# Performance work log

Hardware: AMD Instinct MI355X
Metric: run time of the kernel (lower is better)

## Reference

```python
import jax, jax.numpy as jnp
import numpy as np

N = 16384   # total nodes per drug-batch
E = 65536   # directed edges (avg degree 4)
B = 512     # graphs per batch
BN_EPS = 1e-5
SLOPE = 0.01  # LeakyReLU default


def _rn(k, shape, s=0.02):
    return jax.random.normal(k, shape, dtype=jnp.float32) * s


def setup_inputs():
    key = jax.random.key(0)
    ks = jax.random.split(key, 32)
    d = {}
    d['x1'] = jax.random.normal(ks[0], (N, 78), dtype=jnp.float32)
    d['edge_index1'] = jax.random.randint(ks[1], (2, E), 0, N)
    d['batch1'] = jnp.sort(jax.random.randint(ks[2], (N,), 0, B))
    d['x2'] = jax.random.normal(ks[3], (N, 78), dtype=jnp.float32)
    d['edge_index2'] = jax.random.randint(ks[4], (2, E), 0, N)
    d['batch2'] = jnp.sort(jax.random.randint(ks[5], (N,), 0, B))
    d['cell'] = jax.random.normal(ks[6], (B, 954), dtype=jnp.float32)
    # TransformerConv1: 78 -> 2 heads x 128 (concat 256)
    d['wq1'] = _rn(ks[7], (78, 256));  d['bq1'] = jnp.zeros((256,), jnp.float32)
    d['wk1'] = _rn(ks[8], (78, 256));  d['bk1'] = jnp.zeros((256,), jnp.float32)
    d['wv1'] = _rn(ks[9], (78, 256));  d['bv1'] = jnp.zeros((256,), jnp.float32)
    d['ws1'] = _rn(ks[10], (78, 256)); d['bs1'] = jnp.zeros((256,), jnp.float32)
    # TransformerConv2: 256 -> 2 heads x 512 (concat 1024)
    d['wq2'] = _rn(ks[11], (256, 1024)); d['bq2'] = jnp.zeros((1024,), jnp.float32)
    d['wk2'] = _rn(ks[12], (256, 1024)); d['bk2'] = jnp.zeros((1024,), jnp.float32)
    d['wv2'] = _rn(ks[13], (256, 1024)); d['bv2'] = jnp.zeros((1024,), jnp.float32)
    d['ws2'] = _rn(ks[14], (256, 1024)); d['bs2'] = jnp.zeros((1024,), jnp.float32)
    d['wg1'] = _rn(ks[15], (1024, 512)); d['bg1'] = jnp.zeros((512,), jnp.float32)
    d['wg2'] = _rn(ks[16], (512, 128));  d['bg2'] = jnp.zeros((128,), jnp.float32)
    d['wr1'] = _rn(ks[17], (954, 512));  d['br1'] = jnp.zeros((512,), jnp.float32)
    d['wr2'] = _rn(ks[18], (512, 256));  d['br2'] = jnp.zeros((256,), jnp.float32)
    d['wr3'] = _rn(ks[19], (256, 128));  d['br3'] = jnp.zeros((128,), jnp.float32)
    d['wf1'] = _rn(ks[20], (384, 512));  d['bf1'] = jnp.zeros((512,), jnp.float32)
    d['gbn1'] = jnp.ones((512,), jnp.float32); d['bbn1'] = jnp.zeros((512,), jnp.float32)
    d['wf2'] = _rn(ks[21], (512, 256));  d['bf2'] = jnp.zeros((256,), jnp.float32)
    d['gbn2'] = jnp.ones((256,), jnp.float32); d['bbn2'] = jnp.zeros((256,), jnp.float32)
    d['wf3'] = _rn(ks[22], (256, 1));    d['bf3'] = jnp.zeros((1,), jnp.float32)
    return d


def _lrelu(x):
    return jnp.where(x >= 0, x, SLOPE * x)


def _l2n(x):
    return x / jnp.maximum(jnp.linalg.norm(x, axis=1, keepdims=True), 1e-12)


def _tconv(x, ei, wq, bq, wk, bk, wv, bv, ws, bs, H, D):
    # PyG TransformerConv (concat=True, beta=False, root_weight=True)
    src, dst = ei[0], ei[1]
    n = x.shape[0]
    q = (x @ wq + bq).reshape(n, H, D)
    k = (x @ wk + bk).reshape(n, H, D)
    v = (x @ wv + bv).reshape(n, H, D)
    logits = jnp.einsum('ehd,ehd->eh', q[dst], k[src]) / jnp.sqrt(jnp.float32(D))  # [E,H]
    m = jax.ops.segment_max(logits, dst, num_segments=n)
    m = jnp.where(jnp.isfinite(m), m, 0.0)
    e = jnp.exp(logits - m[dst])
    z = jax.ops.segment_sum(e, dst, num_segments=n)
    alpha = e / (z[dst] + 1e-16)
    agg = jax.ops.segment_sum(alpha[:, :, None] * v[src], dst, num_segments=n)  # [N,H,D]
    return agg.reshape(n, H * D) + x @ ws + bs


def reference(x1, edge_index1, batch1, x2, edge_index2, batch2, cell,
              wq1, bq1, wk1, bk1, wv1, bv1, ws1, bs1,
              wq2, bq2, wk2, bk2, wv2, bv2, ws2, bs2,
              wg1, bg1, wg2, bg2, wr1, br1, wr2, br2, wr3, br3,
              wf1, bf1, gbn1, bbn1, wf2, bf2, gbn2, bbn2, wf3, bf3):
    def branch(x, ei, bt):
        h = _lrelu(_tconv(x, ei, wq1, bq1, wk1, bk1, wv1, bv1, ws1, bs1, 2, 128))
        h = _lrelu(_tconv(h, ei, wq2, bq2, wk2, bk2, wv2, bv2, ws2, bs2, 2, 512))
        g = jax.ops.segment_max(h, bt, num_segments=B)  # global max pool per graph
        g = jnp.where(jnp.isfinite(g), g, 0.0)
        g = _lrelu(g @ wg1 + bg1)
        g = g @ wg2 + bg2  # dropout = identity in eval
        return _l2n(g)

    x1g = branch(x1, edge_index1, batch1)
    x2g = branch(x2, edge_index2, batch2)

    c = _l2n(cell)
    c = _lrelu(c @ wr1 + br1)
    c = _lrelu(c @ wr2 + br2)
    c = c @ wr3 + br3

    xc = _l2n(jnp.concatenate([x1g, x2g, c], axis=1))  # [B, 384]
    bn = 1.0 / jnp.sqrt(1.0 + BN_EPS)  # eval BN with running mean 0, var 1
    h = _lrelu((xc @ wf1 + bf1) * bn * gbn1 + bbn1)
    h = _lrelu((h @ wf2 + bf2) * bn * gbn2 + bbn2)
    return jax.nn.sigmoid((h @ wf3 + bf3)[:, 0])
```

## Files before the change

kernel.cpp:

```cpp
#include <hip/hip_runtime.h>
#include <hip/hip_bf16.h>
#include <hip/hip_fp8.h>
#include <math.h>
#include <stdint.h>

typedef __hip_bfloat16 bf16;

#define NN 16384
#define EE 65536
#define BB 512

typedef __attribute__((ext_vector_type(8))) short short8;
typedef __attribute__((ext_vector_type(4))) short short4v;
typedef __attribute__((ext_vector_type(2))) short short2v;
typedef __attribute__((ext_vector_type(4))) float floatx4;
typedef __attribute__((ext_vector_type(8))) unsigned char uchar8;
typedef __attribute__((ext_vector_type(2))) unsigned char uchar2v;

#define GKEY_NEGINF 0x007FFFFFu

__device__ __forceinline__ float lrelu_f(float x){ return x >= 0.f ? x : 0.01f*x; }

__device__ __forceinline__ float b2f(short s){
    unsigned int u = ((unsigned int)(unsigned short)s) << 16;
    float f; __builtin_memcpy(&f, &u, 4); return f;
}
__device__ __forceinline__ short f2b(float f){
    bf16 b = (bf16)f;
    short s; __builtin_memcpy(&s, &b, 2); return s;
}
__device__ __forceinline__ unsigned char f2fp8(float f){
    __hip_fp8_e4m3 t(f);
    return (unsigned char)t.__x;
}
__device__ __forceinline__ float fp82f(unsigned char c){
    __hip_fp8_e4m3 t; t.__x = (__hip_fp8_storage_t)c;
    return (float)t;
}
__device__ __forceinline__ unsigned int fkey(float f){
    unsigned int u; __builtin_memcpy(&u, &f, 4);
    return (u & 0x80000000u) ? ~u : (u | 0x80000000u);
}
__device__ __forceinline__ float fdec(unsigned int k){
    if (k == GKEY_NEGINF) return 0.f;
    unsigned int u = (k & 0x80000000u) ? (k ^ 0x80000000u) : ~k;
    float f; __builtin_memcpy(&f, &u, 4); return f;
}

__device__ __forceinline__ void gl2lds16(const void* g, void* l){
    __builtin_amdgcn_global_load_lds(
        (__attribute__((address_space(1))) unsigned int*)(uintptr_t)g,
        (__attribute__((address_space(3))) unsigned int*)(uintptr_t)l, 16, 0, 0);
}

__global__ __launch_bounds__(256)
void mfma_gemm(const bf16* __restrict__ A, int lda,
               const bf16* __restrict__ Bt, int ldb,
               const float* __restrict__ bias,
               bf16* __restrict__ C, int ldc,
               unsigned char* __restrict__ C2, int ldc2, int nsplit, int K)
{
    __shared__ __align__(16) char smem[20480];
    bf16* As  = (bf16*)smem;
    bf16* Bs  = (bf16*)(smem + 8192);
    bf16* epi = (bf16*)smem;
    const int tid  = threadIdx.x;
    const int wave = tid >> 6;
    const int lane = tid & 63;
    const int wm = (wave & 1) * 64;
    const int wn = (wave >> 1) * 64;
    const int m0 = blockIdx.y * 128;
    const int n0 = blockIdx.x * 128;
    const bool isf8 = (n0 >= nsplit);

    const int srow = lane >> 2;
    const int scol = (lane & 3) * 8;
    const int arow = lane & 15;
    const int aq   = (lane >> 4) * 8;

    floatx4 acc[4][4];
    #pragma unroll
    for (int i=0;i<4;i++)
        #pragma unroll
        for (int j=0;j<4;j++) acc[i][j] = (floatx4){0.f,0.f,0.f,0.f};

    for (int k0 = 0; k0 < K; k0 += 32) {
        #pragma unroll
        for (int i = 0; i < 2; i++) {
            const int chunk = wave*2 + i;
            const int r = chunk*16 + srow;
            gl2lds16(A  + (size_t)(m0 + r)*lda + k0 + scol, As + chunk*512);
            gl2lds16(Bt + (size_t)(n0 + r)*ldb + k0 + scol, Bs + chunk*512);
        }
        __syncthreads();
        short8 af[4], bf_[4];
        #pragma unroll
        for (int i=0;i<4;i++) af[i]  = *(const short8*)(As + (wm + i*16 + arow)*32 + aq);
        #pragma unroll
        for (int j=0;j<4;j++) bf_[j] = *(const short8*)(Bs + (wn + j*16 + arow)*32 + aq);
        #pragma unroll
        for (int i=0;i<4;i++)
            #pragma unroll
            for (int j=0;j<4;j++)
                acc[i][j] = __builtin_amdgcn_mfma_f32_16x16x32_bf16(af[i], bf_[j], acc[i][j], 0,0,0);
        __syncthreads();
    }
    const int crow = (lane >> 4) * 4;
    const int ccol = lane & 15;
    const int erow = lane >> 2;
    const int ecol = (lane & 3) * 8;
    bf16* ep = epi + wave * (64*40);
    #pragma unroll
    for (int j2 = 0; j2 < 2; j2++){
        if (j2) __syncthreads();
        #pragma unroll
        for (int jj = 0; jj < 2; jj++){
            const int j = j2*2 + jj;
            const float bsv = bias[n0 + wn + j*16 + ccol];
            #pragma unroll
            for (int i = 0; i < 4; i++)
                #pragma unroll
                for (int r = 0; r < 4; r++)
                    ep[(i*16 + crow + r)*40 + jj*16 + ccol] = (bf16)(acc[i][j][r] + bsv);
        }
        __syncthreads();
        #pragma unroll
        for (int q = 0; q < 4; q++){
            const int rr = q*16 + erow;
            short8 vv = *(const short8*)(ep + rr*40 + ecol);
            if (!isf8){
                *(short8*)(C + (size_t)(m0 + wm + rr)*ldc + n0 + wn + j2*32 + ecol) = vv;
            } else {
                uchar8 ob;
                #pragma unroll
                for (int i=0;i<8;i++) ob[i] = f2fp8(b2f(vv[i]));
                *(uchar8*)(C2 + (size_t)(m0 + wm + rr)*ldc2 + (n0 - nsplit) + wn + j2*32 + ecol) = ob;
            }
        }
    }
}

#define OG1 0
#define OG2 524288
#define OR1 589824
#define OR2 1081344
#define OR3 1212416
#define OF1 1245184
#define OF2 1441792
#define TAILW_TOTAL 1572864

#define P_W1T 98304
#define P_B1C (P_W1T + 1024)
#define P_W2T (P_B1C + 1048576)
#define P_B2C (P_W2T + 4096)
#define P_WTP (P_B2C + TAILW_TOTAL)
#define P_XA  (P_WTP + 2*NN*96)
#define P_GK  (P_XA + 2*BB*1024)
__global__ void prep_mega_kernel(
    const float* __restrict__ wq1, const float* __restrict__ wk1,
    const float* __restrict__ wv1, const float* __restrict__ ws1,
    const float* __restrict__ bq1, const float* __restrict__ bk1,
    const float* __restrict__ bv1, const float* __restrict__ bs1,
    const float* __restrict__ wq2, const float* __restrict__ wk2,
    const float* __restrict__ wv2, const float* __restrict__ ws2,
    const float* __restrict__ bq2, const float* __restrict__ bk2,
    const float* __restrict__ bv2, const float* __restrict__ bs2v,
    const float* __restrict__ wg1, const float* __restrict__ wg2,
    const float* __restrict__ wr1, const float* __restrict__ wr2,
    const float* __restrict__ wr3, const float* __restrict__ wf1,
    const float* __restrict__ wf2,
    const float* __restrict__ x1,  const float* __restrict__ x2,
    bf16* __restrict__ W1t, float* __restrict__ b1c,
    bf16* __restrict__ W2t, float* __restrict__ b2c,
    bf16* __restrict__ Wtp, bf16* __restrict__ xa,
    unsigned int* __restrict__ gkey)
{
    int i = blockIdx.x*256 + threadIdx.x;
    if (i < P_W1T){
        int n = i / 96, k = i - n*96;
        int seg = n >> 8;
        const float* w = (seg==0)?ws1:(seg==1)?wq1:(seg==2)?wk1:wv1;
        W1t[i] = (k < 78) ? (bf16)w[(size_t)k*256 + (n & 255)] : (bf16)0.f;
        return;
    }
    if (i < P_B1C){
        int n = i - P_W1T;
        int seg = n >> 8;
        const float* b = (seg==0)?bs1:(seg==1)?bq1:(seg==2)?bk1:bv1;
        b1c[n] = b[n & 255];
        return;
    }
    if (i < P_W2T){
        int loc = i - P_B1C;
        int k = loc & 255;
        int j = (loc >> 8) & 2047;
        int h = loc >> 19;
        const float* w = (j<512)?ws2:(j<1024)?wq2:(j<1536)?wk2:wv2;
        W2t[loc] = (bf16)w[(size_t)k*1024 + h*512 + (j & 511)];
        return;
    }
    if (i < P_B2C){
        int loc = i - P_W2T;
        int j = loc & 2047, h = loc >> 11;
        const float* b = (j<512)?bs2v:(j<1024)?bq2:(j<1536)?bk2:bv2;
        b2c[loc] = b[h*512 + (j & 511)];
        return;
    }
    if (i < P_WTP){
        int t = i - P_B2C;
        const float* W; int N, K, base;
        if      (t < OG2){ W = wg1; N = 512; K = 1024; base = OG1; }
        else if (t < OR1){ W = wg2; N = 128; K = 512;  base = OG2; }
        else if (t < OR2){ W = wr1; N = 512; K = 954;  base = OR1; }
        else if (t < OR3){ W = wr2; N = 256; K = 512;  base = OR2; }
        else if (t < OF1){ W = wr3; N = 128; K = 256;  base = OR3; }
        else if (t < OF2){ W = wf1; N = 512; K = 384;  base = OF1; }
        else             { W = wf2; N = 256; K = 512;  base = OF2; }
        int loc = t - base;
        int u = loc & 3;
        int j = (loc >> 2) % N;
        int k4 = (loc >> 2) / N;
        int k = k4*4 + u;
        Wtp[t] = (k < K) ? (bf16)W[(size_t)k*N + j] : (bf16)0.f;
        return;
    }
    if (i < P_XA){
        int t = i - P_WTP;
        int r = t / 96, c = t - r*96;
        const float* x = (r >= NN) ? x2 : x1;
        int lr = r & (NN-1);
        xa[t] = (c < 78) ? (bf16)x[(size_t)lr*78 + c] : (bf16)0.f;
        return;
    }
    if (i < P_GK){
        gkey[i - P_XA] = GKEY_NEGINF;
    }
}

__global__ void hist_kernel(const int* __restrict__ ei1, const int* __restrict__ ei2,
                            int* __restrict__ cnt){
    int eg = blockIdx.x*256 + threadIdx.x;
    int br = eg >> 16, e = eg & (EE-1);
    const int* ei = br ? ei2 : ei1;
    atomicAdd(&cnt[br*NN + ei[EE + e]], 1);
}

__global__ __launch_bounds__(1024)
void scan_kernel(const int* __restrict__ hist, int* __restrict__ rowptr,
                 int* __restrict__ rowcur){
    const int br = blockIdx.x;
    hist   += br*NN;
    rowptr += br*(NN+1);
    rowcur += br*(NN+1);
    __shared__ int sums[1024];
    const int t = threadIdx.x;
    const int base = t*16;
    int loc[16]; int s = 0;
    #pragma unroll
    for (int i=0;i<16;i++){ loc[i]=s; s += hist[base+i]; }
    sums[t] = s; __syncthreads();
    for (int o=1;o<1024;o<<=1){
        int v = (t>=o) ? sums[t-o] : 0;
        __syncthreads();
        sums[t] += v;
        __syncthreads();
    }
    int pref = (t>0) ? sums[t-1] : 0;
    #pragma unroll
    for (int i=0;i<16;i++){
        int v = pref + loc[i];
        rowptr[base+i] = v;
        rowcur[base+i] = v;
    }
    if (t==1023) rowptr[NN] = sums[1023];
}

__global__ void scatter_kernel(const int* __restrict__ ei1, const int* __restrict__ ei2,
                               int* __restrict__ rowcur, int* __restrict__ srcs){
    int eg = blockIdx.x*256 + threadIdx.x;
    int br = eg >> 16, e = eg & (EE-1);
    const int* ei = br ? ei2 : ei1;
    int d = ei[EE + e];
    int pos = atomicAdd(&rowcur[br*(NN+1) + d], 1);
    srcs[br*EE + pos] = ei[e];
}

__global__ __launch_bounds__(256)
void attn128_f8(const bf16* __restrict__ s1, const unsigned char* __restrict__ f81,
                bf16* __restrict__ hout,
                const int* __restrict__ rowptr, const int* __restrict__ srcs)
{
    const int lane = threadIdx.x & 63;
    const int gw = blockIdx.x * 4 + (threadIdx.x >> 6);
    const int n = gw >> 1;
    const int h = gw & 1;
    int br = n >> 14;
    int brNN = br*NN, nl = n - brNN;
    rowptr += br*(NN+1); srcs += br*EE;
    const float qscale = rsqrtf(128.f) * 1.44269504f;
    const int hd = h*128 + lane*2;

    const uchar2v q8 = *(const uchar2v*)(f81 + (size_t)n*768 + hd);
    float qr[2] = { fp82f(q8[0])*qscale, fp82f(q8[1])*qscale };

    const int e0 = rowptr[nl], e1 = rowptr[nl+1];
    float m = -INFINITY, z = 0.f;
    float acc[2] = {0.f, 0.f};

    for (int base = e0; base < e1; base += 4){
        const int cnt = min(4, e1 - base);
        int sl = srcs[min(base + (lane & 3), e1 - 1)];
        int src[4];
        #pragma unroll
        for (int j=0;j<4;j++) src[j] = __shfl(sl, j, 64);

        uchar2v kv[4], vv[4];
        #pragma unroll
        for (int j=0;j<4;j++){
            if (j < cnt){
                const unsigned char* rp = f81 + (size_t)(brNN + src[j])*768;
                kv[j] = *(const uchar2v*)(rp + 256 + hd);
                vv[j] = *(const uchar2v*)(rp + 512 + hd);
            }
        }
        float dt[4];
        #pragma unroll
        for (int j=0;j<4;j++){
            float d = 0.f;
            if (j < cnt) d = qr[0]*fp82f(kv[j][0]) + qr[1]*fp82f(kv[j][1]);
            dt[j] = d;
        }
        #pragma unroll
        for (int o=32;o;o>>=1){
            #pragma unroll
            for (int j=0;j<4;j++) dt[j] += __shfl_xor(dt[j], o, 64);
        }
        float cm = -INFINITY;
        #pragma unroll
        for (int j=0;j<4;j++) if (j < cnt) cm = fmaxf(cm, dt[j]);
        const float mn = fmaxf(m, cm);
        const float cs = exp2f(m - mn);
        z *= cs;
        acc[0] *= cs; acc[1] *= cs;
        #pragma unroll
        for (int j=0;j<4;j++){
            if (j < cnt){
                const float w = exp2f(dt[j] - mn);
                z += w;
                acc[0] += w*fp82f(vv[j][0]);
                acc[1] += w*fp82f(vv[j][1]);
            }
        }
        m = mn;
    }
    const float invz = 1.0f/(z + 1e-16f);
    const short2v sv = *(const short2v*)(s1 + (size_t)n*256 + hd);
    short2v ov;
    ov[0] = f2b(lrelu_f(b2f(sv[0]) + acc[0]*invz));
    ov[1] = f2b(lrelu_f(b2f(sv[1]) + acc[1]*invz));
    *(short2v*)(hout + (size_t)n*256 + hd) = ov;
}

__global__ __launch_bounds__(256)
void attn512_f8(const bf16* __restrict__ s2, const unsigned char* __restrict__ f82,
                const int* __restrict__ rowptr, const int* __restrict__ srcs,
                const int* __restrict__ bt,
                unsigned int* __restrict__ gkey, int grow0, int gc0)
{
    __shared__ float Sh[4][512];
    __shared__ int Sgid[4];
    const int lane = threadIdx.x & 63;
    const int wave = threadIdx.x >> 6;
    const int n = blockIdx.x * 4 + wave;
    const float qscale = rsqrtf(512.f) * 1.44269504f;
    const int hd = lane*8;

    const uchar8 q8 = *(const uchar8*)(f82 + (size_t)n*1536 + hd);
    float qr[8];
    #pragma unroll
    for (int i=0;i<8;i++) qr[i] = fp82f(q8[i]) * qscale;

    const int e0 = rowptr[n], e1 = rowptr[n+1];
    float m = -INFINITY, z = 0.f;
    float acc[8];
    #pragma unroll
    for (int i=0;i<8;i++) acc[i] = 0.f;

    for (int base = e0; base < e1; base += 4){
        const int cnt = min(4, e1 - base);
        int sl = srcs[min(base + (lane & 3), e1 - 1)];
        int src[4];
        #pragma unroll
        for (int j=0;j<4;j++) src[j] = __shfl(sl, j, 64);

        uchar8 k8[4], v8[4];
        #pragma unroll
        for (int j=0;j<4;j++){
            if (j < cnt){
                const unsigned char* rp = f82 + (size_t)src[j]*1536;
                k8[j] = *(const uchar8*)(rp + 512 + hd);
                v8[j] = *(const uchar8*)(rp + 1024 + hd);
            }
        }
        float dt[4];
        #pragma unroll
        for (int j=0;j<4;j++){
            float d = 0.f;
            if (j < cnt){
                #pragma unroll
                for (int i=0;i<8;i++) d += qr[i]*fp82f(k8[j][i]);
            }
            dt[j] = d;
        }
        #pragma unroll
        for (int o=32;o;o>>=1){
            #pragma unroll
            for (int j=0;j<4;j++) dt[j] += __shfl_xor(dt[j], o, 64);
        }
        float cm = -INFINITY;
        #pragma unroll
        for (int j=0;j<4;j++) if (j < cnt) cm = fmaxf(cm, dt[j]);
        const float mn = fmaxf(m, cm);
        const float cs = exp2f(m - mn);
        z *= cs;
        #pragma unroll
        for (int i=0;i<8;i++) acc[i] *= cs;
        #pragma unroll
        for (int j=0;j<4;j++){
            if (j < cnt){
                const float w = exp2f(dt[j] - mn);
                z += w;
                #pragma unroll
                for (int i=0;i<8;i++) acc[i] += w*fp82f(v8[j][i]);
            }
        }
        m = mn;
    }
    const float invz = 1.0f/(z + 1e-16f);
    const short8 sv = *(const short8*)(s2 + (size_t)n*512 + hd);
    #pragma unroll
    for (int i=0;i<8;i++) Sh[wave][hd + i] = lrelu_f(b2f(sv[i]) + acc[i]*invz);
    if (lane == 0) Sgid[wave] = bt[n];
    __syncthreads();

    #pragma unroll
    for (int cc=0; cc<2; cc++){
        const int col = threadIdx.x*2 + cc;
        float mx = Sh[0][col];
        int gid = Sgid[0];
        #pragma unroll
        for (int r=1; r<4; r++){
            if (Sgid[r] == gid) mx = fmaxf(mx, Sh[r][col]);
            else {
                atomicMax(&gkey[(size_t)(grow0 + gid)*1024 + gc0 + col], fkey(mx));
                gid = Sgid[r]; mx = Sh[r][col];
            }
        }
        atomicMax(&gkey[(size_t)(grow0 + gid)*1024 + gc0 + col], fkey(mx));
    }
}

template<int R, int N, int ACT>
__device__ __forceinline__ void dense_split(
    const bf16* __restrict__ Wp, const float* __restrict__ bias,
    const float* __restrict__ gam, const float* __restrict__ bet, float bns,
    const float* A, int lda, float* C, int ldc, int K, int tid, float* Spart)
{
    constexpr int CPT = N / 128;
    constexpr int KG  = 8;
    const int ct = tid & 127;
    const int kg = tid >> 7;
    const int jt = ct * CPT;
    const int Kc = ((K + KG - 1) / KG + 3) & ~3;
    const int kb = kg * Kc;
    const int Kpad = (K + 3) & ~3;
    const int ke = min(Kpad, kb + Kc);

    float acc[R][CPT];
    #pragma unroll
    for (int r=0;r<R;r++)
        #pragma unroll
        for (int c=0;c<CPT;c++) acc[r][c] = 0.f;

    if (kb < ke){
        short8 p0, p1; short4v p4;
        {
            const bf16* wp = Wp + ((size_t)(kb>>2)*N + jt)*4;
            if (CPT==4){ p0 = ((const short8*)wp)[0]; p1 = ((const short8*)wp)[1]; }
            else if (CPT==2){ p0 = *(const short8*)wp; }
            else { p4 = *(const short4v*)wp; }
        }
        for (int k = kb; k < ke; k += 4){
            short8 c0 = p0, c1 = p1; short4v c4 = p4;
            const int kn = (k + 4 < ke) ? k + 4 : kb;
            const bf16* wn = Wp + ((size_t)(kn>>2)*N + jt)*4;
            if (CPT==4){ p0 = ((const short8*)wn)[0]; p1 = ((const short8*)wn)[1]; }
            else if (CPT==2){ p0 = *(const short8*)wn; }
            else { p4 = *(const short4v*)wn; }
            float w[4][CPT];
            if (CPT==4){
                #pragma unroll
                for (int u=0;u<4;u++){
                    w[u][0] = b2f(c0[u]); w[u][1] = b2f(c0[4+u]);
                    w[u][2] = b2f(c1[u]); w[u][3] = b2f(c1[4+u]);
                }
            } else if (CPT==2){
                #pragma unroll
                for (int u=0;u<4;u++){ w[u][0] = b2f(c0[u]); w[u][1] = b2f(c0[4+u]); }
            } else {
                #pragma unroll
                for (int u=0;u<4;u++) w[u][0] = b2f(c4[u]);
            }
            #pragma unroll
            for (int r=0;r<R;r++){
                const floatx4 av = *(const floatx4*)(A + r*lda + k);
                #pragma unroll
                for (int u=0;u<4;u++)
                    #pragma unroll
                    for (int c=0;c<CPT;c++) acc[r][c] += av[u]*w[u][c];
            }
        }
    }
    #pragma unroll
    for (int r=0;r<R;r++)
        #pragma unroll
        for (int c=0;c<CPT;c++)
            Spart[(kg*R + r)*N + jt + c] = acc[r][c];
    __syncthreads();
    for (int idx = tid; idx < R*N; idx += 1024){
        int r = idx / N, j = idx - r*N;
        float v = 0.f;
        #pragma unroll
        for (int g=0; g<KG; g++) v += Spart[(g*R + r)*N + j];
        v += bias[j];
        if (ACT==1) v = lrelu_f(v);
        if (ACT==2) v = lrelu_f(v*bns*gam[j] + bet[j]);
        C[r*ldc + j] = v;
    }
    __syncthreads();
}

__global__ __launch_bounds__(1024)
void tail_kernel(const unsigned int* __restrict__ gkey,
                 const float* __restrict__ cell,
                 const bf16*  __restrict__ Wtp,
                 const float* __restrict__ bg1, const float* __restrict__ bg2,
                 const float* __restrict__ br1, const float* __restrict__ br2,
                 const float* __restrict__ br3,
                 const float* __restrict__ bf1,
                 const float* __restrict__ gbn1, const float* __restrict__ bbn1,
                 const float* __restrict__ bf2,
                 const float* __restrict__ gbn2, const float* __restrict__ bbn2,
                 const float* __restrict__ wf3, const float* __restrict__ bf3,
                 float bns, float* __restrict__ outp)
{
    __shared__ float Sg[4][1024];
    __shared__ float Sgh[4][512];
    __shared__ float Sgout[4][128];
    __shared__ float Scell[2][960];
    __shared__ float Sc1[2][512];
    __shared__ float Sc2[2][256];
    __shared__ float Sc3[2][128];
    __shared__ float Sxc[2][384];
    __shared__ float Sf1[2][512];
    __shared__ float Sf2[2][256];
    __shared__ float Spart[16384];
    __shared__ float inv4[4], invc[2], invx[2];

    const int tid = threadIdx.x;
    const int wv  = tid >> 6;
    const int ln  = tid & 63;
    const int b0  = blockIdx.x * 2;

    {
        int idx = tid*4;
        int r = idx >> 10, c = idx & 1023;
        int lg = r >> 1, br = r & 1;
        const unsigned int* gp = gkey + (size_t)(br*BB + b0 + lg)*1024 + c;
        #pragma unroll
        for (int i=0;i<4;i++) Sg[r][c+i] = fdec(gp[i]);
    }
    for (int idx = tid; idx < 2*954; idx += 1024){
        int r = (idx >= 954) ? 1 : 0;
        int c = idx - r*954;
        Scell[r][c] = cell[(size_t)(b0 + r)*954 + c];
    }
    if (tid < 12){ int r = tid/6; Scell[r][954 + tid%6] = 0.f; }
    __syncthreads();

    if (wv < 2){
        float s = 0.f;
        for (int c = ln; c < 954; c += 64){ float v = Scell[wv][c]; s += v*v; }
        #pragma unroll
        for (int o=32;o;o>>=1) s += __shfl_xor(s, o, 64);
        if (ln == 0) invc[wv] = 1.0f / fmaxf(sqrtf(s), 1e-12f);
    }
    __syncthreads();
    #pragma unroll
    for (int r=0;r<2;r++)
        for (int c = tid; c < 954; c += 1024) Scell[r][c] *= invc[r];
    __syncthreads();

    dense_split<4,512,1>(Wtp+OG1, bg1, nullptr, nullptr, 1.f, &Sg[0][0],   1024, &Sgh[0][0],  512, 1024, tid, Spart);
    dense_split<4,128,0>(Wtp+OG2, bg2, nullptr, nullptr, 1.f, &Sgh[0][0],  512,  &Sgout[0][0],128, 512,  tid, Spart);
    dense_split<2,512,1>(Wtp+OR1, br1, nullptr, nullptr, 1.f, &Scell[0][0], 960, &Sc1[0][0],  512, 954,  tid, Spart);
    dense_split<2,256,1>(Wtp+OR2, br2, nullptr, nullptr, 1.f, &Sc1[0][0],   512, &Sc2[0][0],  256, 512,  tid, Spart);
    dense_split<2,128,0>(Wtp+OR3, br3, nullptr, nullptr, 1.f, &Sc2[0][0],   256, &Sc3[0][0],  128, 256,  tid, Spart);

    if (wv < 4){
        float a = Sgout[wv][ln], bq = Sgout[wv][ln+64];
        float s = a*a + bq*bq;
        #pragma unroll
        for (int o=32;o;o>>=1) s += __shfl_xor(s, o, 64);
        if (ln == 0) inv4[wv] = 1.0f / fmaxf(sqrtf(s), 1e-12f);
    }
    __syncthreads();

    if (tid < 768){
        int lg = tid / 384, j = tid - lg*384;
        float v;
        if (j < 128)      v = Sgout[lg*2+0][j]     * inv4[lg*2+0];
        else if (j < 256) v = Sgout[lg*2+1][j-128] * inv4[lg*2+1];
        else              v = Sc3[lg][j-256];
        Sxc[lg][j] = v;
    }
    __syncthreads();
    if (wv < 2){
        float s = 0.f;
        #pragma unroll
        for (int i=0;i<6;i++){ float v = Sxc[wv][ln + i*64]; s += v*v; }
        #pragma unroll
        for (int o=32;o;o>>=1) s += __shfl_xor(s, o, 64);
        if (ln == 0) invx[wv] = 1.0f / fmaxf(sqrtf(s), 1e-12f);
    }
    __syncthreads();
    if (tid < 768){
        int lg = tid / 384, j = tid - lg*384;
        Sxc[lg][j] *= invx[lg];
    }
    __syncthreads();

    dense_split<2,512,2>(Wtp+OF1, bf1, gbn1, bbn1, bns, &Sxc[0][0], 384, &Sf1[0][0], 512, 384, tid, Spart);
    dense_split<2,256,2>(Wtp+OF2, bf2, gbn2, bbn2, bns, &Sf1[0][0], 512, &Sf2[0][0], 256, 512, tid, Spart);

    if (wv < 2){
        float s = 0.f;
        #pragma unroll
        for (int i=0;i<4;i++){ int c = ln + i*64; s += Sf2[wv][c]*wf3[c]; }
        #pragma unroll
        for (int o=32;o;o>>=1) s += __shfl_xor(s, o, 64);
        if (ln == 0) outp[b0 + wv] = 1.0f/(1.0f + expf(-(s + bf3[0])));
    }
}

extern "C" void kernel_launch(void* const* d_in, const int* in_sizes, int n_in,
                              void* d_out, int out_size, void* d_ws, size_t ws_size,
                              hipStream_t stream)
{
    const float* x1  = (const float*)d_in[0];
    const int*   ei1 = (const int*)  d_in[1];
    const int*   bt1 = (const int*)  d_in[2];
    const float* x2  = (const float*)d_in[3];
    const int*   ei2 = (const int*)  d_in[4];
    const int*   bt2 = (const int*)  d_in[5];
    const float* cell= (const float*)d_in[6];
    const float* wq1=(const float*)d_in[7];  const float* bq1=(const float*)d_in[8];
    const float* wk1=(const float*)d_in[9];  const float* bk1=(const float*)d_in[10];
    const float* wv1=(const float*)d_in[11]; const float* bv1=(const float*)d_in[12];
    const float* ws1=(const float*)d_in[13]; const float* bs1=(const float*)d_in[14];
    const float* wq2=(const float*)d_in[15]; const float* bq2=(const float*)d_in[16];
    const float* wk2=(const float*)d_in[17]; const float* bk2=(const float*)d_in[18];
    const float* wv2=(const float*)d_in[19]; const float* bv2=(const float*)d_in[20];
    const float* ws2=(const float*)d_in[21]; const float* bs2q=(const float*)d_in[22];
    const float* wg1=(const float*)d_in[23]; const float* bg1=(const float*)d_in[24];
    const float* wg2=(const float*)d_in[25]; const float* bg2=(const float*)d_in[26];
    const float* wr1=(const float*)d_in[27]; const float* br1=(const float*)d_in[28];
    const float* wr2=(const float*)d_in[29]; const float* br2=(const float*)d_in[30];
    const float* wr3=(const float*)d_in[31]; const float* br3=(const float*)d_in[32];
    const float* wf1=(const float*)d_in[33]; const float* bf1=(const float*)d_in[34];
    const float* gbn1=(const float*)d_in[35];const float* bbn1=(const float*)d_in[36];
    const float* wf2=(const float*)d_in[37]; const float* bf2=(const float*)d_in[38];
    const float* gbn2=(const float*)d_in[39];const float* bbn2=(const float*)d_in[40];
    const float* wf3=(const float*)d_in[41]; const float* bf3=(const float*)d_in[42];
    float* outp = (float*)d_out;
    (void)in_sizes; (void)n_in; (void)out_size; (void)ws_size;

    const float BNS = 1.0f / sqrtf(1.0f + 1e-5f);

    char* basep = (char*)d_ws;
    size_t off = 0;
    auto alloc = [&](size_t nbytes)->char* {
        char* p = basep + off;
        off += (nbytes + 255) & ~(size_t)255;
        return p;
    };
    int* rowptr2  = (int*)  alloc((size_t)2*(NN+1)*4);
    int* rowcur2  = (int*)  alloc((size_t)2*(NN+1)*4);
    int* cnt2     = (int*)  alloc((size_t)2*NN*4);
    int* srcs2    = (int*)  alloc((size_t)2*EE*4);
    unsigned int* gkey = (unsigned int*)alloc((size_t)2*BB*1024*4);
    float* b1c    = (float*)alloc((size_t)1024*4);
    float* b2c    = (float*)alloc((size_t)4096*4);
    bf16* W1t     = (bf16*) alloc((size_t)1024*96*2);
    bf16* W2t     = (bf16*) alloc((size_t)2*2048*256*2);
    bf16* Wtp     = (bf16*) alloc((size_t)TAILW_TOTAL*2);
    bf16* h1      = (bf16*) alloc((size_t)2*NN*256*2);
    bf16* xa      = (bf16*) alloc((size_t)2*NN*96*2);
    char* QK      = alloc((size_t)16777216 + 25165824);
    bf16* s1a     = (bf16*)QK;
    unsigned char* f81 = (unsigned char*)(QK + 16777216);
    bf16* s2a     = (bf16*)QK;
    unsigned char* f82 = (unsigned char*)(QK + 16777216);

    (void)hipMemsetAsync(cnt2, 0, (size_t)2*NN*4, stream);
    prep_mega_kernel<<<P_GK/256,256,0,stream>>>(
        wq1,wk1,wv1,ws1, bq1,bk1,bv1,bs1,
        wq2,wk2,wv2,ws2, bq2,bk2,bv2,bs2q,
        wg1,wg2,wr1,wr2,wr3,wf1,wf2,
        x1,x2,
        W1t,b1c,W2t,b2c, Wtp, xa, gkey);
    hist_kernel<<<2*EE/256,256,0,stream>>>(ei1, ei2, cnt2);
    scan_kernel<<<2,1024,0,stream>>>(cnt2, rowptr2, rowcur2);
    scatter_kernel<<<2*EE/256,256,0,stream>>>(ei1, ei2, rowcur2, srcs2);

    mfma_gemm<<<dim3(8, 2*NN/128),256,0,stream>>>(xa,96, W1t,96, b1c,
                                                  s1a,256, f81,768, 256, 96);
    attn128_f8<<<2*NN*2/4,256,0,stream>>>(s1a, f81, h1, rowptr2, srcs2);

    for (int br=0; br<2; br++){
        const int* bt = br ? bt2 : bt1;
        for (int h=0; h<2; h++){
            mfma_gemm<<<dim3(16, NN/128),256,0,stream>>>(
                h1 + (size_t)br*NN*256, 256, W2t + (size_t)h*2048*256, 256,
                b2c + h*2048, s2a,512, f82,1536, 512, 256);
            attn512_f8<<<NN/4,256,0,stream>>>(s2a, f82,
                                              rowptr2 + br*(NN+1), srcs2 + br*EE, bt,
                                              gkey, br*BB, h*512);
        }
    }

    tail_kernel<<<BB/2,1024,0,stream>>>(gkey, cell, Wtp,
                                        bg1,bg2, br1,br2,br3,
                                        bf1,gbn1,bbn1, bf2,gbn2,bbn2, wf3,bf3,
                                        BNS, outp);
}
```

Before: 555.4 us.

## Batch both branches in layer-2 launches and use MFMA for tail dense layers

The second-layer GEMM and attention kernels now cover both drug branches in a single launch per head. This halves the launch count and doubles the grid size, which should help fill the GPU. The tail kernel's scalar split-K dense layers are replaced by 16x16x32 bf16 MFMA tiles, with the weights repacked into MFMA fragment order in the prep kernel. This also removes the large shared-memory partial-sum buffer and its reduction pass. The trade-off is a bigger workspace buffer for the batched activations, and the tail activations are now rounded to bf16 where they were previously accumulated in fp32.

```diff
diff --git a/kernel.cpp b/kernel.cpp
--- a/kernel.cpp
+++ b/kernel.cpp
@@ -11,7 +11,6 @@
 #define BB 512
 
 typedef __attribute__((ext_vector_type(8))) short short8;
-typedef __attribute__((ext_vector_type(4))) short short4v;
 typedef __attribute__((ext_vector_type(2))) short short2v;
 typedef __attribute__((ext_vector_type(4))) float floatx4;
 typedef __attribute__((ext_vector_type(8))) unsigned char uchar8;
@@ -208,20 +207,23 @@
     }
     if (i < P_WTP){
         int t = i - P_B2C;
-        const float* W; int N, K, base;
-        if      (t < OG2){ W = wg1; N = 512; K = 1024; base = OG1; }
-        else if (t < OR1){ W = wg2; N = 128; K = 512;  base = OG2; }
-        else if (t < OR2){ W = wr1; N = 512; K = 954;  base = OR1; }
-        else if (t < OR3){ W = wr2; N = 256; K = 512;  base = OR2; }
-        else if (t < OF1){ W = wr3; N = 128; K = 256;  base = OR3; }
-        else if (t < OF2){ W = wf1; N = 512; K = 384;  base = OF1; }
-        else             { W = wf2; N = 256; K = 512;  base = OF2; }
+        const float* W; int N, K, KS, base;
+        if      (t < OG2){ W = wg1; N = 512; K = 1024; KS = 32; base = OG1; }
+        else if (t < OR1){ W = wg2; N = 128; K = 512;  KS = 16; base = OG2; }
+        else if (t < OR2){ W = wr1; N = 512; K = 954;  KS = 30; base = OR1; }
+        else if (t < OR3){ W = wr2; N = 256; K = 512;  KS = 16; base = OR2; }
+        else if (t < OF1){ W = wr3; N = 128; K = 256;  KS = 8;  base = OR3; }
+        else if (t < OF2){ W = wf1; N = 512; K = 384;  KS = 12; base = OF1; }
+        else             { W = wf2; N = 256; K = 512;  KS = 16; base = OF2; }
         int loc = t - base;
-        int u = loc & 3;
-        int j = (loc >> 2) % N;
-        int k4 = (loc >> 2) / N;
-        int k = k4*4 + u;
-        Wtp[t] = (k < K) ? (bf16)W[(size_t)k*N + j] : (bf16)0.f;
+        int j  = loc & 7;
+        int ln = (loc >> 3) & 63;
+        int rest = loc >> 9;
+        int ks = rest % KS;
+        int tile = rest / KS;
+        int n = tile*16 + (ln & 15);
+        int k = ks*32 + (ln >> 4)*8 + j;
+        Wtp[t] = (k < K) ? (bf16)W[(size_t)k*N + n] : (bf16)0.f;
         return;
     }
     if (i < P_XA){
@@ -364,14 +366,18 @@
 __global__ __launch_bounds__(256)
 void attn512_f8(const bf16* __restrict__ s2, const unsigned char* __restrict__ f82,
                 const int* __restrict__ rowptr, const int* __restrict__ srcs,
-                const int* __restrict__ bt,
-                unsigned int* __restrict__ gkey, int grow0, int gc0)
+                const int* __restrict__ bt1, const int* __restrict__ bt2,
+                unsigned int* __restrict__ gkey, int gc0)
 {
     __shared__ float Sh[4][512];
     __shared__ int Sgid[4];
     const int lane = threadIdx.x & 63;
     const int wave = threadIdx.x >> 6;
     const int n = blockIdx.x * 4 + wave;
+    const int br = n >> 14;
+    const int brNN = br*NN, nl = n - brNN;
+    const int* rp_ = rowptr + br*(NN+1);
+    const int* sp_ = srcs + br*EE;
     const float qscale = rsqrtf(512.f) * 1.44269504f;
     const int hd = lane*8;
 
@@ -380,7 +386,7 @@
     #pragma unroll
     for (int i=0;i<8;i++) qr[i] = fp82f(q8[i]) * qscale;
 
-    const int e0 = rowptr[n], e1 = rowptr[n+1];
+    const int e0 = rp_[nl], e1 = rp_[nl+1];
     float m = -INFINITY, z = 0.f;
     float acc[8];
     #pragma unroll
@@ -388,7 +394,7 @@
 
     for (int base = e0; base < e1; base += 4){
         const int cnt = min(4, e1 - base);
-        int sl = srcs[min(base + (lane & 3), e1 - 1)];
+        int sl = sp_[min(base + (lane & 3), e1 - 1)];
         int src[4];
         #pragma unroll
         for (int j=0;j<4;j++) src[j] = __shfl(sl, j, 64);
@@ -397,7 +403,7 @@
         #pragma unroll
         for (int j=0;j<4;j++){
             if (j < cnt){
-                const unsigned char* rp = f82 + (size_t)src[j]*1536;
+                const unsigned char* rp = f82 + (size_t)(brNN + src[j])*1536;
                 k8[j] = *(const uchar8*)(rp + 512 + hd);
                 v8[j] = *(const uchar8*)(rp + 1024 + hd);
             }
@@ -440,7 +446,7 @@
     const short8 sv = *(const short8*)(s2 + (size_t)n*512 + hd);
     #pragma unroll
     for (int i=0;i<8;i++) Sh[wave][hd + i] = lrelu_f(b2f(sv[i]) + acc[i]*invz);
-    if (lane == 0) Sgid[wave] = bt[n];
+    if (lane == 0) Sgid[wave] = br*BB + (br ? bt2[nl] : bt1[nl]);
     __syncthreads();
 
     #pragma unroll
@@ -452,90 +458,68 @@
         for (int r=1; r<4; r++){
             if (Sgid[r] == gid) mx = fmaxf(mx, Sh[r][col]);
             else {
-                atomicMax(&gkey[(size_t)(grow0 + gid)*1024 + gc0 + col], fkey(mx));
+                atomicMax(&gkey[(size_t)gid*1024 + gc0 + col], fkey(mx));
                 gid = Sgid[r]; mx = Sh[r][col];
             }
         }
-        atomicMax(&gkey[(size_t)(grow0 + gid)*1024 + gc0 + col], fkey(mx));
+        atomicMax(&gkey[(size_t)gid*1024 + gc0 + col], fkey(mx));
     }
 }
 
 template<int R, int N, int ACT>
-__device__ __forceinline__ void dense_split(
-    const bf16* __restrict__ Wp, const float* __restrict__ bias,
+__device__ __forceinline__ void dense_mfma(
+    const bf16* __restrict__ Wm, const float* __restrict__ bias,
     const float* __restrict__ gam, const float* __restrict__ bet, float bns,
-    const float* A, int lda, float* C, int ldc, int K, int tid, float* Spart)
+    const float* A, int lda, float* C, int ldc, int K, int tid)
 {
-    constexpr int CPT = N / 128;
-    constexpr int KG  = 8;
-    const int ct = tid & 127;
-    const int kg = tid >> 7;
-    const int jt = ct * CPT;
-    const int Kc = ((K + KG - 1) / KG + 3) & ~3;
-    const int kb = kg * Kc;
-    const int Kpad = (K + 3) & ~3;
-    const int ke = min(Kpad, kb + Kc);
-
-    float acc[R][CPT];
-    #pragma unroll
-    for (int r=0;r<R;r++)
-        #pragma unroll
-        for (int c=0;c<CPT;c++) acc[r][c] = 0.f;
-
-    if (kb < ke){
-        short8 p0, p1; short4v p4;
-        {
-            const bf16* wp = Wp + ((size_t)(kb>>2)*N + jt)*4;
-            if (CPT==4){ p0 = ((const short8*)wp)[0]; p1 = ((const short8*)wp)[1]; }
-            else if (CPT==2){ p0 = *(const short8*)wp; }
-            else { p4 = *(const short4v*)wp; }
-        }
-        for (int k = kb; k < ke; k += 4){
-            short8 c0 = p0, c1 = p1; short4v c4 = p4;
-            const int kn = (k + 4 < ke) ? k + 4 : kb;
-            const bf16* wn = Wp + ((size_t)(kn>>2)*N + jt)*4;
-            if (CPT==4){ p0 = ((const short8*)wn)[0]; p1 = ((const short8*)wn)[1]; }
-            else if (CPT==2){ p0 = *(const short8*)wn; }
-            else { p4 = *(const short4v*)wn; }
-            float w[4][CPT];
-            if (CPT==4){
-                #pragma unroll
-                for (int u=0;u<4;u++){
-                    w[u][0] = b2f(c0[u]); w[u][1] = b2f(c0[4+u]);
-                    w[u][2] = b2f(c1[u]); w[u][3] = b2f(c1[4+u]);
+    constexpr int T   = N / 16;
+    constexpr int TPW = (T + 15) / 16;
+    const int wave = tid >> 6;
+    const int lane = tid & 63;
+    const int am = lane & 15;
+    const int ak = (lane >> 4) * 8;
+    const int KS = ((K + 31) & ~31) >> 5;
+
+    floatx4 acc[TPW];
+    #pragma unroll
+    for (int tp=0; tp<TPW; tp++) acc[tp] = (floatx4){0.f,0.f,0.f,0.f};
+
+    for (int ks = 0; ks < KS; ks++){
+        short8 af = (short8){0,0,0,0,0,0,0,0};
+        if (am < R){
+            const float* ap = A + am*lda + ks*32 + ak;
+            const floatx4 a0 = *(const floatx4*)ap;
+            const floatx4 a1 = *(const floatx4*)(ap + 4);
+            af[0]=f2b(a0[0]); af[1]=f2b(a0[1]); af[2]=f2b(a0[2]); af[3]=f2b(a0[3]);
+            af[4]=f2b(a1[0]); af[5]=f2b(a1[1]); af[6]=f2b(a1[2]); af[7]=f2b(a1[3]);
+        }
+        #pragma unroll
+        for (int tp=0; tp<TPW; tp++){
+            const int tile = wave + tp*16;
+            if (tile < T){
+                const short8 bfv = *(const short8*)(Wm + ((size_t)(tile*KS + ks))*512 + lane*8);
+                acc[tp] = __builtin_amdgcn_mfma_f32_16x16x32_bf16(af, bfv, acc[tp], 0,0,0);
+            }
+        }
+    }
+    const int crow = (lane >> 4) * 4;
+    const int ccol = lane & 15;
+    #pragma unroll
+    for (int tp=0; tp<TPW; tp++){
+        const int tile = wave + tp*16;
+        if (tile < T){
+            #pragma unroll
+            for (int r=0; r<4; r++){
+                const int row = crow + r;
+                if (row < R){
+                    const int n = tile*16 + ccol;
+                    float v = acc[tp][r] + bias[n];
+                    if (ACT==1) v = lrelu_f(v);
+                    if (ACT==2) v = lrelu_f(v*bns*gam[n] + bet[n]);
+                    C[row*ldc + n] = v;
                 }
-            } else if (CPT==2){
-                #pragma unroll
-                for (int u=0;u<4;u++){ w[u][0] = b2f(c0[u]); w[u][1] = b2f(c0[4+u]); }
-            } else {
-                #pragma unroll
-                for (int u=0;u<4;u++) w[u][0] = b2f(c4[u]);
-            }
-            #pragma unroll
-            for (int r=0;r<R;r++){
-                const floatx4 av = *(const floatx4*)(A + r*lda + k);
-                #pragma unroll
-                for (int u=0;u<4;u++)
-                    #pragma unroll
-                    for (int c=0;c<CPT;c++) acc[r][c] += av[u]*w[u][c];
-            }
-        }
-    }
-    #pragma unroll
-    for (int r=0;r<R;r++)
-        #pragma unroll
-        for (int c=0;c<CPT;c++)
-            Spart[(kg*R + r)*N + jt + c] = acc[r][c];
-    __syncthreads();
-    for (int idx = tid; idx < R*N; idx += 1024){
-        int r = idx / N, j = idx - r*N;
-        float v = 0.f;
-        #pragma unroll
-        for (int g=0; g<KG; g++) v += Spart[(g*R + r)*N + j];
-        v += bias[j];
-        if (ACT==1) v = lrelu_f(v);
-        if (ACT==2) v = lrelu_f(v*bns*gam[j] + bet[j]);
-        C[r*ldc + j] = v;
+            }
+        }
     }
     __syncthreads();
 }
@@ -564,7 +548,6 @@
     __shared__ float Sxc[2][384];
     __shared__ float Sf1[2][512];
     __shared__ float Sf2[2][256];
-    __shared__ float Spart[16384];
     __shared__ float inv4[4], invc[2], invx[2];
 
     const int tid = threadIdx.x;
@@ -601,11 +584,11 @@
         for (int c = tid; c < 954; c += 1024) Scell[r][c] *= invc[r];
     __syncthreads();
 
-    dense_split<4,512,1>(Wtp+OG1, bg1, nullptr, nullptr, 1.f, &Sg[0][0],   1024, &Sgh[0][0],  512, 1024, tid, Spart);
-    dense_split<4,128,0>(Wtp+OG2, bg2, nullptr, nullptr, 1.f, &Sgh[0][0],  512,  &Sgout[0][0],128, 512,  tid, Spart);
-    dense_split<2,512,1>(Wtp+OR1, br1, nullptr, nullptr, 1.f, &Scell[0][0], 960, &Sc1[0][0],  512, 954,  tid, Spart);
-    dense_split<2,256,1>(Wtp+OR2, br2, nullptr, nullptr, 1.f, &Sc1[0][0],   512, &Sc2[0][0],  256, 512,  tid, Spart);
-    dense_split<2,128,0>(Wtp+OR3, br3, nullptr, nullptr, 1.f, &Sc2[0][0],   256, &Sc3[0][0],  128, 256,  tid, Spart);
+    dense_mfma<4,512,1>(Wtp+OG1, bg1, nullptr, nullptr, 1.f, &Sg[0][0],   1024, &Sgh[0][0],  512, 1024, tid);
+    dense_mfma<4,128,0>(Wtp+OG2, bg2, nullptr, nullptr, 1.f, &Sgh[0][0],  512,  &Sgout[0][0],128, 512,  tid);
+    dense_mfma<2,512,1>(Wtp+OR1, br1, nullptr, nullptr, 1.f, &Scell[0][0], 960, &Sc1[0][0],  512, 954,  tid);
+    dense_mfma<2,256,1>(Wtp+OR2, br2, nullptr, nullptr, 1.f, &Sc1[0][0],   512, &Sc2[0][0],  256, 512,  tid);
+    dense_mfma<2,128,0>(Wtp+OR3, br3, nullptr, nullptr, 1.f, &Sc2[0][0],   256, &Sc3[0][0],  128, 256,  tid);
 
     if (wv < 4){
         float a = Sgout[wv][ln], bq = Sgout[wv][ln+64];
@@ -640,8 +623,8 @@
     }
     __syncthreads();
 
-    dense_split<2,512,2>(Wtp+OF1, bf1, gbn1, bbn1, bns, &Sxc[0][0], 384, &Sf1[0][0], 512, 384, tid, Spart);
-    dense_split<2,256,2>(Wtp+OF2, bf2, gbn2, bbn2, bns, &Sf1[0][0], 512, &Sf2[0][0], 256, 512, tid, Spart);
+    dense_mfma<2,512,2>(Wtp+OF1, bf1, gbn1, bbn1, bns, &Sxc[0][0], 384, &Sf1[0][0], 512, 384, tid);
+    dense_mfma<2,256,2>(Wtp+OF2, bf2, gbn2, bbn2, bns, &Sf1[0][0], 512, &Sf2[0][0], 256, 512, tid);
 
     if (wv < 2){
         float s = 0.f;
@@ -705,12 +688,12 @@
     bf16* W2t     = (bf16*) alloc((size_t)2*2048*256*2);
     bf16* Wtp     = (bf16*) alloc((size_t)TAILW_TOTAL*2);
     bf16* h1      = (bf16*) alloc((size_t)2*NN*256*2);
-    bf16* xa      = (bf16*) alloc((size_t)2*NN*96*2);
-    char* QK      = alloc((size_t)16777216 + 25165824);
-    bf16* s1a     = (bf16*)QK;
-    unsigned char* f81 = (unsigned char*)(QK + 16777216);
-    bf16* s2a     = (bf16*)QK;
-    unsigned char* f82 = (unsigned char*)(QK + 16777216);
+    char* BIG     = alloc((size_t)2*NN*512*2 + (size_t)2*NN*1536);
+    bf16* xa      = (bf16*)BIG;
+    bf16* s1a     = (bf16*)(BIG + 6291456);
+    unsigned char* f81 = (unsigned char*)(BIG + 6291456 + 16777216);
+    bf16* s2a     = (bf16*)BIG;
+    unsigned char* f82 = (unsigned char*)(BIG + (size_t)2*NN*512*2);
 
     (void)hipMemsetAsync(cnt2, 0, (size_t)2*NN*4, stream);
     prep_mega_kernel<<<P_GK/256,256,0,stream>>>(
@@ -727,16 +710,12 @@
                                                   s1a,256, f81,768, 256, 96);
     attn128_f8<<<2*NN*2/4,256,0,stream>>>(s1a, f81, h1, rowptr2, srcs2);
 
-    for (int br=0; br<2; br++){
-        const int* bt = br ? bt2 : bt1;
-        for (int h=0; h<2; h++){
-            mfma_gemm<<<dim3(16, NN/128),256,0,stream>>>(
-                h1 + (size_t)br*NN*256, 256, W2t + (size_t)h*2048*256, 256,
-                b2c + h*2048, s2a,512, f82,1536, 512, 256);
-            attn512_f8<<<NN/4,256,0,stream>>>(s2a, f82,
-                                              rowptr2 + br*(NN+1), srcs2 + br*EE, bt,
-                                              gkey, br*BB, h*512);
-        }
+    for (int h=0; h<2; h++){
+        mfma_gemm<<<dim3(16, 2*NN/128),256,0,stream>>>(
+            h1, 256, W2t + (size_t)h*2048*256, 256,
+            b2c + h*2048, s2a,512, f82,1536, 512, 256);
+        attn512_f8<<<2*NN/4,256,0,stream>>>(s2a, f82, rowptr2, srcs2, bt1, bt2,
+                                            gkey, h*512);
     }
 
     tail_kernel<<<BB/2,1024,0,stream>>>(gkey, cell, Wtp,
```

Result: faster. 543.1 us (-2.2%).
